# Performance work log

Hardware: AMD Instinct MI355X
Metric: run time of the kernel (lower is better)

## Reference

```python
import jax, jax.numpy as jnp
import numpy as np

B, N, E, H = 16, 768, 1024, 16  # batch == heads so mask[i] (head-indexed, as in the source) is valid
D = E // H
MASK_P = 0.1
NEG = jnp.float32(-1e16)


def setup_inputs() -> dict:
    key = jax.random.key(0)
    ks = jax.random.split(key, 8)
    query = jax.random.normal(ks[0], (B, N, E), jnp.float32)
    key_t = jax.random.normal(ks[1], (B, N, E), jnp.float32)
    value = jax.random.normal(ks[2], (B, N, E), jnp.float32)
    u = jax.random.uniform(ks[3], (B, N))
    mask = jnp.where(u < MASK_P, -jnp.inf, 0.0).astype(jnp.float32)
    # per-head Linear(head_dim, head_dim, bias=False) weights, stacked over heads: (H, out=D, in=D)
    Wq = jax.random.normal(ks[4], (H, D, D), jnp.float32) * (1.0 / np.sqrt(D))
    Wk = jax.random.normal(ks[5], (H, D, D), jnp.float32) * (1.0 / np.sqrt(D))
    Wv = jax.random.normal(ks[6], (H, D, D), jnp.float32) * (1.0 / np.sqrt(D))
    Wf = jax.random.normal(ks[7], (E, E), jnp.float32) * (1.0 / np.sqrt(E))
    return {"query": query, "key": key_t, "value": value, "mask": mask,
            "Wq": Wq, "Wk": Wk, "Wv": Wv, "Wf": Wf}


def reference(query, key, value, mask, Wq, Wk, Wv, Wf):
    b, n, e = query.shape
    h = Wq.shape[0]
    d = e // h
    q = query.reshape(b, n, h, d)
    k = key.reshape(b, n, h, d)
    v = value.reshape(b, n, h, d)
    # per-head nn.Linear: x @ W[i].T  (W: (H, out, in))
    qh = jnp.einsum('bnhd,hed->bnhe', q, Wq)
    kh = jnp.einsum('bnhd,hed->bnhe', k, Wk)
    vh = jnp.einsum('bnhd,hed->bnhe', v, Wv)
    # scaled QK^T: divide by embed_size**0.5 (NOT head_dim) as in the source
    scores = jnp.einsum('bqhd,bkhd->bhqk', qh, kh) / jnp.sqrt(jnp.float32(e))  # (B,H,N,N)
    # faithful quirk: mask row selected by HEAD index i -> same additive mask for all batches
    bad = jnp.isneginf(mask)[:h]                      # (H, N)
    add = jnp.where(bad[:, :, None] | bad[:, None, :], NEG, jnp.float32(0.0))  # (H,N,N): row/col blanked
    probs = jax.nn.softmax(scores + add[None], axis=-1)
    attn = jnp.einsum('bhqk,bkhd->bqhd', probs, vh)   # (B,N,H,D)
    out = attn.reshape(b, n, e) @ Wf.T
    return out
```

## Files before the change

### kernel.cpp

```cpp
#include <hip/hip_runtime.h>

#define B_ 16
#define N_ 768
#define E_ 1024
#define H_ 16
#define D_ 64

typedef __bf16 bf16x8 __attribute__((ext_vector_type(8)));
typedef float f32x4 __attribute__((ext_vector_type(4)));
typedef unsigned short ushort8 __attribute__((ext_vector_type(8)));
typedef unsigned short ushort4v __attribute__((ext_vector_type(4)));
typedef unsigned int uint2v __attribute__((ext_vector_type(2)));
typedef unsigned int uint4v __attribute__((ext_vector_type(4)));

__device__ __forceinline__ unsigned short f2bf(float x) {
  unsigned u = __builtin_bit_cast(unsigned, x);
  u += 0x7FFFu + ((u >> 16) & 1u);
  return (unsigned short)(u >> 16);
}

__device__ __forceinline__ unsigned cvtpk(float lo, float hi) {
  unsigned r;
  asm("v_cvt_pk_bf16_f32 %0, %1, %2" : "=v"(r) : "v"(lo), "v"(hi));
  return r;
}

__device__ __forceinline__ f32x4 mfma16(ushort8 a, ushort8 b, f32x4 c) {
  return __builtin_amdgcn_mfma_f32_16x16x32_bf16(
      __builtin_bit_cast(bf16x8, a), __builtin_bit_cast(bf16x8, b), c, 0, 0, 0);
}

__global__ __launch_bounds__(256) void wf_kernel(const float* __restrict__ Wf,
                                                 unsigned short* __restrict__ Wfb) {
  size_t g = (size_t)blockIdx.x * 256 + threadIdx.x;
  float4 xv = *(const float4*)&Wf[g * 4];
  ushort4v s;
  s[0] = f2bf(xv.x); s[1] = f2bf(xv.y); s[2] = f2bf(xv.z); s[3] = f2bf(xv.w);
  *(ushort4v*)&Wfb[g * 4] = s;
}

__global__ __launch_bounds__(256) void proj_kernel(
    const float* __restrict__ q, const float* __restrict__ k, const float* __restrict__ v,
    const float* __restrict__ Wq, const float* __restrict__ Wk, const float* __restrict__ Wv,
    unsigned short* __restrict__ Qh, unsigned short* __restrict__ Kh,
    unsigned short* __restrict__ Vt) {
  const int nt = blockIdx.x % 12;
  const int bh = blockIdx.x / 12;
  const int b = bh >> 4, h = bh & 15;
  const int tid = threadIdx.x;
  const int w = tid >> 6, l = tid & 63;
  const int l16 = l & 15, lg = l >> 4;

  __shared__ __align__(16) unsigned short Xs[3][64][72];
  __shared__ __align__(16) unsigned short Ws[3][64][72];

  const float* xin[3] = {q, k, v};
  const float* win[3] = {Wq, Wk, Wv};

#pragma unroll
  for (int m = 0; m < 3; ++m) {
    const float* xp = xin[m];
#pragma unroll
    for (int i = 0; i < 4; ++i) {
      int flat = i * 256 + tid;
      int row = flat >> 4;
      int c4 = (flat & 15) * 4;
      float4 xv = *(const float4*)&xp[((size_t)(b * N_ + nt * 64 + row)) * E_ + h * 64 + c4];
      ushort4v s;
      s[0] = f2bf(xv.x); s[1] = f2bf(xv.y); s[2] = f2bf(xv.z); s[3] = f2bf(xv.w);
      *(ushort4v*)&Xs[m][row][c4] = s;
    }
    const float* wp = win[m] + (size_t)h * 4096;
#pragma unroll
    for (int i = 0; i < 4; ++i) {
      int flat = i * 256 + tid;
      int row = flat >> 4;
      int c4 = (flat & 15) * 4;
      float4 wv = *(const float4*)&wp[row * 64 + c4];
      ushort4v s;
      s[0] = f2bf(wv.x); s[1] = f2bf(wv.y); s[2] = f2bf(wv.z); s[3] = f2bf(wv.w);
      *(ushort4v*)&Ws[m][row][c4] = s;
    }
  }
  __syncthreads();

  f32x4 vacc[4];
#pragma unroll
  for (int m = 0; m < 3; ++m) {
    f32x4 acc[4] = {};
#pragma unroll
    for (int kc = 0; kc < 2; ++kc) {
      ushort8 a = *(const ushort8*)&Xs[m][w * 16 + l16][kc * 32 + lg * 8];
#pragma unroll
      for (int eg = 0; eg < 4; ++eg) {
        ushort8 bf = *(const ushort8*)&Ws[m][eg * 16 + l16][kc * 32 + lg * 8];
        acc[eg] = mfma16(a, bf, acc[eg]);
      }
    }
    if (m == 2) {
#pragma unroll
      for (int eg = 0; eg < 4; ++eg) vacc[eg] = acc[eg];
    } else {
      unsigned short* op = (m == 0) ? Qh : Kh;
#pragma unroll
      for (int eg = 0; eg < 4; ++eg)
#pragma unroll
        for (int r = 0; r < 4; ++r)
          op[((size_t)(b * H_ + h) * N_ + nt * 64 + w * 16 + lg * 4 + r) * 64 + eg * 16 + l16] =
              f2bf(acc[eg][r]);
    }
  }

  __syncthreads();
#pragma unroll
  for (int eg = 0; eg < 4; ++eg) {
    uint2v pk;
    pk[0] = cvtpk(vacc[eg][0], vacc[eg][1]);
    pk[1] = cvtpk(vacc[eg][2], vacc[eg][3]);
    *(uint2v*)&Xs[0][eg * 16 + l16][w * 16 + lg * 4] = pk;
  }
  __syncthreads();
#pragma unroll
  for (int i = 0; i < 2; ++i) {
    int row = i * 32 + (tid >> 3), c8 = (tid & 7) * 8;
    *(ushort8*)&Vt[((size_t)bh * 64 + row) * N_ + nt * 64 + c8] =
        *(const ushort8*)&Xs[0][row][c8];
  }
}

__global__ __launch_bounds__(256, 4) void attn_kernel(
    const unsigned short* __restrict__ Qh, const unsigned short* __restrict__ Kh,
    const unsigned short* __restrict__ Vt, const float* __restrict__ mask,
    unsigned short* __restrict__ attnO) {
  const int bid = blockIdx.x;
  const int logical = (bid & 7) * 192 + (bid >> 3);
  const int qt = logical % 6;
  const int bh = logical / 6;
  const int b = bh >> 4, h = bh & 15;
  const int tid = threadIdx.x;
  const int w = tid >> 6, l = tid & 63;
  const int l16 = l & 15, lg = l >> 4;

  __shared__ __align__(16) unsigned short Ks[64][72];
  __shared__ __align__(16) unsigned short Vs[64][72];
  __shared__ __align__(16) unsigned short Ps[4][32][72];
  __shared__ float badk[N_];

  const size_t baseK = (size_t)bh * N_ * 64;
  const size_t baseV = (size_t)bh * 64 * N_;
  const int qrow0 = qt * 128 + w * 32;

  for (int i = tid; i < N_; i += 256) badk[i] = (mask[h * N_ + i] < -1e30f) ? 1.f : 0.f;

  ushort8 bQ[2][2];
#pragma unroll
  for (int qs = 0; qs < 2; ++qs)
#pragma unroll
    for (int kc = 0; kc < 2; ++kc)
      bQ[qs][kc] = *(const ushort8*)&Qh[((size_t)bh * N_ + qrow0 + qs * 16 + l16) * 64 +
                                        kc * 32 + lg * 8];
  float bqf[2];
#pragma unroll
  for (int qs = 0; qs < 2; ++qs)
    bqf[qs] = (mask[h * N_ + qrow0 + qs * 16 + l16] < -1e30f) ? 1.f : 0.f;

  const int srow = tid >> 3;
  const int sc8 = (tid & 7) * 8;

  uint4v kreg[2], vreg[2];
#pragma unroll
  for (int i = 0; i < 2; ++i) {
    int row = i * 32 + srow;
    kreg[i] = *(const uint4v*)&Kh[baseK + (size_t)row * 64 + sc8];
    vreg[i] = *(const uint4v*)&Vt[baseV + (size_t)row * N_ + sc8];
  }
  __syncthreads();
#pragma unroll
  for (int i = 0; i < 2; ++i) {
    int row = i * 32 + srow;
    *(ushort8*)&Ks[row][sc8] = __builtin_bit_cast(ushort8, kreg[i]);
    *(ushort8*)&Vs[row][sc8] = __builtin_bit_cast(ushort8, vreg[i]);
  }
  __syncthreads();

  f32x4 oacc[2][4] = {};
  float l_part[2] = {0.f, 0.f};

  for (int kt = 0; kt < 12; ++kt) {
    if (kt < 11) {
#pragma unroll
      for (int i = 0; i < 2; ++i) {
        int row = i * 32 + srow;
        kreg[i] = *(const uint4v*)&Kh[baseK + (size_t)((kt + 1) * 64 + row) * 64 + sc8];
        vreg[i] = *(const uint4v*)&Vt[baseV + (size_t)row * N_ + (kt + 1) * 64 + sc8];
      }
    }

#pragma unroll
    for (int cg = 0; cg < 4; ++cg) {
      f32x4 st[2] = {};
#pragma unroll
      for (int kc = 0; kc < 2; ++kc) {
        ushort8 aK = *(const ushort8*)&Ks[cg * 16 + l16][kc * 32 + lg * 8];
#pragma unroll
        for (int qs = 0; qs < 2; ++qs) st[qs] = mfma16(aK, bQ[qs][kc], st[qs]);
      }
      f32x4 bk4 = *(const f32x4*)&badk[kt * 64 + cg * 16 + lg * 4];
#pragma unroll
      for (int qs = 0; qs < 2; ++qs) {
        float p[4];
#pragma unroll
        for (int r = 0; r < 4; ++r) {
          float t = st[qs][r] * 0.03125f;
          t = (bk4[r] > 0.f) ? -1e16f : t;
          t = (bqf[qs] > 0.f) ? 0.f : t;
          p[r] = __expf(t);
          l_part[qs] += p[r];
        }
        uint2v pk;
        pk[0] = cvtpk(p[0], p[1]);
        pk[1] = cvtpk(p[2], p[3]);
        *(uint2v*)&Ps[w][qs * 16 + l16][cg * 16 + lg * 4] = pk;
      }
    }

#pragma unroll
    for (int kc = 0; kc < 2; ++kc) {
      ushort8 ap[2];
#pragma unroll
      for (int qs = 0; qs < 2; ++qs)
        ap[qs] = *(const ushort8*)&Ps[w][qs * 16 + l16][kc * 32 + lg * 8];
#pragma unroll
      for (int dg = 0; dg < 4; ++dg) {
        ushort8 bv = *(const ushort8*)&Vs[dg * 16 + l16][kc * 32 + lg * 8];
#pragma unroll
        for (int qs = 0; qs < 2; ++qs) oacc[qs][dg] = mfma16(ap[qs], bv, oacc[qs][dg]);
      }
    }

    __syncthreads();
    if (kt < 11) {
#pragma unroll
      for (int i = 0; i < 2; ++i) {
        int row = i * 32 + srow;
        *(ushort8*)&Ks[row][sc8] = __builtin_bit_cast(ushort8, kreg[i]);
        *(ushort8*)&Vs[row][sc8] = __builtin_bit_cast(ushort8, vreg[i]);
      }
    }
    __syncthreads();
  }

#pragma unroll
  for (int qs = 0; qs < 2; ++qs) {
    float s = l_part[qs];
    s += __shfl_xor(s, 16);
    s += __shfl_xor(s, 32);
#pragma unroll
    for (int r = 0; r < 4; ++r) {
      float dnm = __shfl(s, lg * 4 + r);
      float inv = 1.f / dnm;
      int qg = qrow0 + qs * 16 + lg * 4 + r;
      size_t orow = ((size_t)b * N_ + qg) * E_ + h * 64;
#pragma unroll
      for (int dg = 0; dg < 4; ++dg)
        attnO[orow + dg * 16 + l16] = f2bf(oacc[qs][dg][r] * inv);
    }
  }
}

__global__ __launch_bounds__(256) void gemm_kernel(const unsigned short* __restrict__ A,
                                                   const unsigned short* __restrict__ Bm,
                                                   float* __restrict__ out) {
  const int be = blockIdx.x & 7;
  const int bm = blockIdx.x >> 3;
  const int tid = threadIdx.x;
  const int w = tid >> 6, l = tid & 63;
  const int l16 = l & 15, lg = l >> 4;
  const int wm = w >> 1, wn = w & 1;

  __shared__ __align__(16) unsigned short As[128][72];
  __shared__ __align__(16) unsigned short Bs[128][72];

  f32x4 acc[4][4] = {};
  const int m0 = bm * 128, e0 = be * 128;

  for (int kk = 0; kk < 16; ++kk) {
    __syncthreads();
#pragma unroll
    for (int i = 0; i < 4; ++i) {
      int flat = i * 256 + tid;
      int row = flat >> 3;
      int c8 = (flat & 7) * 8;
      *(ushort8*)&As[row][c8] = *(const ushort8*)&A[(size_t)(m0 + row) * E_ + kk * 64 + c8];
      *(ushort8*)&Bs[row][c8] = *(const ushort8*)&Bm[(size_t)(e0 + row) * E_ + kk * 64 + c8];
    }
    __syncthreads();
#pragma unroll
    for (int kc = 0; kc < 2; ++kc) {
      ushort8 a[4], bf[4];
#pragma unroll
      for (int i = 0; i < 4; ++i)
        a[i] = *(const ushort8*)&As[wm * 64 + i * 16 + l16][kc * 32 + lg * 8];
#pragma unroll
      for (int j = 0; j < 4; ++j)
        bf[j] = *(const ushort8*)&Bs[wn * 64 + j * 16 + l16][kc * 32 + lg * 8];
#pragma unroll
      for (int i = 0; i < 4; ++i)
#pragma unroll
        for (int j = 0; j < 4; ++j) acc[i][j] = mfma16(a[i], bf[j], acc[i][j]);
    }
  }

#pragma unroll
  for (int i = 0; i < 4; ++i)
#pragma unroll
    for (int j = 0; j < 4; ++j)
#pragma unroll
      for (int r = 0; r < 4; ++r)
        out[(size_t)(m0 + wm * 64 + i * 16 + lg * 4 + r) * E_ + e0 + wn * 64 + j * 16 + l16] =
            acc[i][j][r];
}

extern "C" void kernel_launch(void* const* d_in, const int* in_sizes, int n_in,
                              void* d_out, int out_size, void* d_ws, size_t ws_size,
                              hipStream_t stream) {
  const float* q = (const float*)d_in[0];
  const float* k = (const float*)d_in[1];
  const float* v = (const float*)d_in[2];
  const float* mask = (const float*)d_in[3];
  const float* Wq = (const float*)d_in[4];
  const float* Wk = (const float*)d_in[5];
  const float* Wv = (const float*)d_in[6];
  const float* Wf = (const float*)d_in[7];
  float* out = (float*)d_out;

  const size_t PH = (size_t)B_ * H_ * N_ * D_;
  unsigned short* Qh = (unsigned short*)d_ws;
  unsigned short* Kh = Qh + PH;
  unsigned short* Vt = Kh + PH;
  unsigned short* attn = Vt + PH;
  unsigned short* Wfb = attn + PH;

  wf_kernel<<<(E_ * E_) / (256 * 4), 256, 0, stream>>>(Wf, Wfb);
  proj_kernel<<<B_ * H_ * (N_ / 64), 256, 0, stream>>>(q, k, v, Wq, Wk, Wv, Qh, Kh, Vt);
  attn_kernel<<<B_ * H_ * (N_ / 128), 256, 0, stream>>>(Qh, Kh, Vt, mask, attn);
  gemm_kernel<<<(B_ * N_ / 128) * (E_ / 128), 256, 0, stream>>>(attn, Wfb, out);
}
```

Before: 160.7 us.

## Keep P in registers via permlane swaps, double-buffer K/V, prefetch GEMM tiles

In the attention kernel the K/V shared tiles are double-buffered, which cuts the per-step synchronisation from two barriers to one. The softmax probabilities no longer go through shared memory: they are packed to bf16 and rearranged across lanes with permlane32/16 swap instructions so they can feed the PV MFMA directly. The exponential now uses the hardware exp2 with a folded scale and an additive mask bias. The output GEMM gains register prefetch of the next K-slice tiles, and the attention occupancy hint is dropped, so register pressure may rise.

```diff
diff --git a/kernel.cpp b/kernel.cpp
--- a/kernel.cpp
+++ b/kernel.cpp
@@ -22,6 +22,12 @@
 __device__ __forceinline__ unsigned cvtpk(float lo, float hi) {
   unsigned r;
   asm("v_cvt_pk_bf16_f32 %0, %1, %2" : "=v"(r) : "v"(lo), "v"(hi));
+  return r;
+}
+
+__device__ __forceinline__ float fexp2(float x) {
+  float r;
+  asm("v_exp_f32 %0, %1" : "=v"(r) : "v"(x));
   return r;
 }
 
@@ -128,7 +134,7 @@
   }
 }
 
-__global__ __launch_bounds__(256, 4) void attn_kernel(
+__global__ __launch_bounds__(256) void attn_kernel(
     const unsigned short* __restrict__ Qh, const unsigned short* __restrict__ Kh,
     const unsigned short* __restrict__ Vt, const float* __restrict__ mask,
     unsigned short* __restrict__ attnO) {
@@ -141,16 +147,17 @@
   const int w = tid >> 6, l = tid & 63;
   const int l16 = l & 15, lg = l >> 4;
 
-  __shared__ __align__(16) unsigned short Ks[64][72];
-  __shared__ __align__(16) unsigned short Vs[64][72];
-  __shared__ __align__(16) unsigned short Ps[4][32][72];
-  __shared__ float badk[N_];
+  __shared__ __align__(16) unsigned short Ks[2][64][72];
+  __shared__ __align__(16) unsigned short Vs[2][64][72];
+  __shared__ __align__(16) float addk[N_];
 
   const size_t baseK = (size_t)bh * N_ * 64;
   const size_t baseV = (size_t)bh * 64 * N_;
   const int qrow0 = qt * 128 + w * 32;
-
-  for (int i = tid; i < N_; i += 256) badk[i] = (mask[h * N_ + i] < -1e30f) ? 1.f : 0.f;
+  const float C2 = 0.04508422f;
+
+  for (int i = tid; i < N_; i += 256)
+    addk[i] = (mask[h * N_ + i] < -1e30f) ? -1000.0f : 0.0f;
 
   ushort8 bQ[2][2];
 #pragma unroll
@@ -166,88 +173,95 @@
 
   const int srow = tid >> 3;
   const int sc8 = (tid & 7) * 8;
+  const unsigned short* kb = Kh + baseK + (size_t)srow * 64 + sc8;
+  const unsigned short* vb = Vt + baseV + (size_t)srow * N_ + sc8;
 
   uint4v kreg[2], vreg[2];
 #pragma unroll
   for (int i = 0; i < 2; ++i) {
-    int row = i * 32 + srow;
-    kreg[i] = *(const uint4v*)&Kh[baseK + (size_t)row * 64 + sc8];
-    vreg[i] = *(const uint4v*)&Vt[baseV + (size_t)row * N_ + sc8];
-  }
-  __syncthreads();
+    kreg[i] = *(const uint4v*)(kb + (size_t)i * 32 * 64);
+    vreg[i] = *(const uint4v*)(vb + (size_t)i * 32 * N_);
+  }
 #pragma unroll
   for (int i = 0; i < 2; ++i) {
-    int row = i * 32 + srow;
-    *(ushort8*)&Ks[row][sc8] = __builtin_bit_cast(ushort8, kreg[i]);
-    *(ushort8*)&Vs[row][sc8] = __builtin_bit_cast(ushort8, vreg[i]);
-  }
-  __syncthreads();
+    *(ushort8*)&Ks[0][i * 32 + srow][sc8] = __builtin_bit_cast(ushort8, kreg[i]);
+    *(ushort8*)&Vs[0][i * 32 + srow][sc8] = __builtin_bit_cast(ushort8, vreg[i]);
+  }
 
   f32x4 oacc[2][4] = {};
   float l_part[2] = {0.f, 0.f};
 
   for (int kt = 0; kt < 12; ++kt) {
+    __syncthreads();
+    const int cur = kt & 1;
+
     if (kt < 11) {
 #pragma unroll
       for (int i = 0; i < 2; ++i) {
-        int row = i * 32 + srow;
-        kreg[i] = *(const uint4v*)&Kh[baseK + (size_t)((kt + 1) * 64 + row) * 64 + sc8];
-        vreg[i] = *(const uint4v*)&Vt[baseV + (size_t)row * N_ + (kt + 1) * 64 + sc8];
+        kreg[i] = *(const uint4v*)(kb + (size_t)(kt + 1) * 4096 + (size_t)i * 2048);
+        vreg[i] = *(const uint4v*)(vb + (size_t)(kt + 1) * 64 + (size_t)i * 32 * N_);
+      }
+    }
+
+    f32x4 st[4][2] = {};
+#pragma unroll
+    for (int kc = 0; kc < 2; ++kc) {
+#pragma unroll
+      for (int cg = 0; cg < 4; ++cg) {
+        ushort8 aK = *(const ushort8*)&Ks[cur][cg * 16 + l16][kc * 32 + lg * 8];
+        st[cg][0] = mfma16(aK, bQ[0][kc], st[cg][0]);
+        st[cg][1] = mfma16(aK, bQ[1][kc], st[cg][1]);
       }
     }
 
 #pragma unroll
     for (int cg = 0; cg < 4; ++cg) {
-      f32x4 st[2] = {};
-#pragma unroll
-      for (int kc = 0; kc < 2; ++kc) {
-        ushort8 aK = *(const ushort8*)&Ks[cg * 16 + l16][kc * 32 + lg * 8];
-#pragma unroll
-        for (int qs = 0; qs < 2; ++qs) st[qs] = mfma16(aK, bQ[qs][kc], st[qs]);
-      }
-      f32x4 bk4 = *(const f32x4*)&badk[kt * 64 + cg * 16 + lg * 4];
+      f32x4 ak4 = *(const f32x4*)&addk[kt * 64 + cg * 16 + lg * 4];
 #pragma unroll
       for (int qs = 0; qs < 2; ++qs) {
-        float p[4];
 #pragma unroll
         for (int r = 0; r < 4; ++r) {
-          float t = st[qs][r] * 0.03125f;
-          t = (bk4[r] > 0.f) ? -1e16f : t;
-          t = (bqf[qs] > 0.f) ? 0.f : t;
-          p[r] = __expf(t);
-          l_part[qs] += p[r];
+          float t = __builtin_fmaf(st[cg][qs][r], C2, ak4[r]);
+          float e = fexp2(t);
+          float p = (bqf[qs] > 0.f) ? 1.0f : e;
+          l_part[qs] += p;
+          st[cg][qs][r] = p;
         }
-        uint2v pk;
-        pk[0] = cvtpk(p[0], p[1]);
-        pk[1] = cvtpk(p[2], p[3]);
-        *(uint2v*)&Ps[w][qs * 16 + l16][cg * 16 + lg * 4] = pk;
-      }
-    }
-
-#pragma unroll
-    for (int kc = 0; kc < 2; ++kc) {
-      ushort8 ap[2];
-#pragma unroll
-      for (int qs = 0; qs < 2; ++qs)
-        ap[qs] = *(const ushort8*)&Ps[w][qs * 16 + l16][kc * 32 + lg * 8];
+      }
+    }
+
+#pragma unroll
+    for (int kcP = 0; kcP < 2; ++kcP) {
+      ushort8 pa[2];
+#pragma unroll
+      for (int qs = 0; qs < 2; ++qs) {
+        unsigned a0 = cvtpk(st[2 * kcP][qs][0], st[2 * kcP][qs][1]);
+        unsigned b0 = cvtpk(st[2 * kcP][qs][2], st[2 * kcP][qs][3]);
+        unsigned a1 = cvtpk(st[2 * kcP + 1][qs][0], st[2 * kcP + 1][qs][1]);
+        unsigned b1 = cvtpk(st[2 * kcP + 1][qs][2], st[2 * kcP + 1][qs][3]);
+        asm("v_permlane32_swap_b32 %0, %1" : "+v"(a0), "+v"(a1));
+        asm("v_permlane16_swap_b32 %0, %1" : "+v"(a0), "+v"(a1));
+        asm("v_permlane32_swap_b32 %0, %1" : "+v"(b0), "+v"(b1));
+        asm("v_permlane16_swap_b32 %0, %1" : "+v"(b0), "+v"(b1));
+        uint4v pk;
+        pk[0] = a0; pk[1] = b0; pk[2] = a1; pk[3] = b1;
+        pa[qs] = __builtin_bit_cast(ushort8, pk);
+      }
 #pragma unroll
       for (int dg = 0; dg < 4; ++dg) {
-        ushort8 bv = *(const ushort8*)&Vs[dg * 16 + l16][kc * 32 + lg * 8];
-#pragma unroll
-        for (int qs = 0; qs < 2; ++qs) oacc[qs][dg] = mfma16(ap[qs], bv, oacc[qs][dg]);
-      }
-    }
-
-    __syncthreads();
+        ushort8 bv = *(const ushort8*)&Vs[cur][dg * 16 + l16][kcP * 32 + lg * 8];
+        oacc[0][dg] = mfma16(pa[0], bv, oacc[0][dg]);
+        oacc[1][dg] = mfma16(pa[1], bv, oacc[1][dg]);
+      }
+    }
+
     if (kt < 11) {
 #pragma unroll
       for (int i = 0; i < 2; ++i) {
-        int row = i * 32 + srow;
-        *(ushort8*)&Ks[row][sc8] = __builtin_bit_cast(ushort8, kreg[i]);
-        *(ushort8*)&Vs[row][sc8] = __builtin_bit_cast(ushort8, vreg[i]);
-      }
-    }
-    __syncthreads();
+        *(ushort8*)&Ks[cur ^ 1][i * 32 + srow][sc8] = __builtin_bit_cast(ushort8, kreg[i]);
+        *(ushort8*)&Vs[cur ^ 1][i * 32 + srow][sc8] = __builtin_bit_cast(ushort8, vreg[i]);
+      }
+    }
   }
 
 #pragma unroll
@@ -283,18 +297,32 @@
 
   f32x4 acc[4][4] = {};
   const int m0 = bm * 128, e0 = be * 128;
+  const int srow = tid >> 3, sc8 = (tid & 7) * 8;
+  const unsigned short* Ab = A + (size_t)(m0 + srow) * E_ + sc8;
+  const unsigned short* Bb = Bm + (size_t)(e0 + srow) * E_ + sc8;
+
+  uint4v ar[4], br[4];
+#pragma unroll
+  for (int i = 0; i < 4; ++i) {
+    ar[i] = *(const uint4v*)(Ab + (size_t)i * 32 * E_);
+    br[i] = *(const uint4v*)(Bb + (size_t)i * 32 * E_);
+  }
 
   for (int kk = 0; kk < 16; ++kk) {
     __syncthreads();
 #pragma unroll
     for (int i = 0; i < 4; ++i) {
-      int flat = i * 256 + tid;
-      int row = flat >> 3;
-      int c8 = (flat & 7) * 8;
-      *(ushort8*)&As[row][c8] = *(const ushort8*)&A[(size_t)(m0 + row) * E_ + kk * 64 + c8];
-      *(ushort8*)&Bs[row][c8] = *(const ushort8*)&Bm[(size_t)(e0 + row) * E_ + kk * 64 + c8];
+      *(ushort8*)&As[i * 32 + srow][sc8] = __builtin_bit_cast(ushort8, ar[i]);
+      *(ushort8*)&Bs[i * 32 + srow][sc8] = __builtin_bit_cast(ushort8, br[i]);
     }
     __syncthreads();
+    if (kk < 15) {
+#pragma unroll
+      for (int i = 0; i < 4; ++i) {
+        ar[i] = *(const uint4v*)(Ab + (size_t)i * 32 * E_ + (kk + 1) * 64);
+        br[i] = *(const uint4v*)(Bb + (size_t)i * 32 * E_ + (kk + 1) * 64);
+      }
+    }
 #pragma unroll
     for (int kc = 0; kc < 2; ++kc) {
       ushort8 a[4], bf[4];
```

Measured after the change: 158.2 us. No clear change (-1.5%).
